# Performance work log

Hardware: AMD Instinct MI355X
Metric: run time of the kernel (lower is better)

The kernel has to match this reference:

```python
import jax, jax.numpy as jnp
import numpy as np

D_MODEL = 1024
HEADS = 16
HEAD_DIM = D_MODEL // HEADS


def setup_inputs() -> dict:
    key = jax.random.key(0)
    ks = jax.random.split(key, 6)
    B, S, D = 2, 2048, D_MODEL
    scale = 1.0 / np.sqrt(D)
    x = jax.random.normal(ks[0], (B, S, D), dtype=jnp.float32)
    mask = jax.random.randint(ks[1], (B, S), 0, 2, dtype=jnp.int32)
    Wq = jax.random.normal(ks[2], (D, D), dtype=jnp.float32) * scale
    Wk = jax.random.normal(ks[3], (D, D), dtype=jnp.float32) * scale
    Wv = jax.random.normal(ks[4], (D, D), dtype=jnp.float32) * scale
    Wp = jax.random.normal(ks[5], (D, D), dtype=jnp.float32) * scale
    zb = jnp.zeros((D,), dtype=jnp.float32)
    return {"x": x, "mask": mask, "Wq": Wq, "bq": zb, "Wk": Wk, "bk": zb,
            "Wv": Wv, "bv": zb, "Wp": Wp, "bp": zb}


def reference(x, mask, Wq, bq, Wk, bk, Wv, bv, Wp, bp):
    B, S, D = x.shape
    H, Dh = HEADS, HEAD_DIM

    def split_heads(t):  # [B,S,D] -> [B,H,S,Dh]
        return t.reshape(B, S, H, Dh).transpose(0, 2, 1, 3)

    q = split_heads(x @ Wq + bq)
    k = split_heads(x @ Wk + bk)
    v = split_heads(x @ Wv + bv)

    att = jnp.einsum('bhqd,bhkd->bhqk', q, k) / jnp.sqrt(jnp.float32(Dh))
    # key-padding mask: [B,S] -> [B,1,1,S]; masked positions -> -inf
    m = (mask[:, None, None, :] != 0)
    att = jnp.where(m, att, -jnp.inf)
    att = jax.nn.softmax(att, axis=-1)
    # rows that were fully masked produce NaN -> zero them (masked_fill(isnan, 0))
    att = jnp.where(jnp.isnan(att), 0.0, att)

    y = jnp.einsum('bhqk,bhkd->bhqd', att, v)  # [B,H,S,Dh]
    y = y.transpose(0, 2, 1, 3).reshape(B, S, D)
    return y @ Wp + bp
```

## Files before the change

### kernel.cpp

```cpp
#include <hip/hip_runtime.h>
#include <math.h>

#define D_MODEL 1024
#define HEADS 16
#define HEAD_DIM 64
#define SEQ 2048
#define BATCH 2
#define KVT 64
#define QTILE 128
#define SCALE_Q 0.18033688f

typedef __attribute__((ext_vector_type(8))) short bf16x8;
typedef __attribute__((ext_vector_type(4))) float f32x4;
typedef __attribute__((ext_vector_type(16))) float f32x16;

__device__ __forceinline__ short f2bf(float f) {
    union { float f; unsigned u; } v; v.f = f;
    unsigned r = (v.u + 0x7FFFu + ((v.u >> 16) & 1u)) >> 16;
    return (short)r;
}

__device__ __forceinline__ unsigned cvt_pk_bf16(float lo, float hi) {
    unsigned r;
    asm("v_cvt_pk_bf16_f32 %0, %1, %2" : "=v"(r) : "v"(lo), "v"(hi));
    return r;
}

__device__ __forceinline__ float fexp2(float x) {
    float r;
    asm("v_exp_f32 %0, %1" : "=v"(r) : "v"(x));
    return r;
}

__global__ __launch_bounds__(256) void prep(
    const float* __restrict__ x, const float* __restrict__ Wq,
    const float* __restrict__ Wk, const float* __restrict__ Wv,
    const float* __restrict__ Wp, const int* __restrict__ mask,
    short* __restrict__ xb, short* __restrict__ Wqkvt,
    short* __restrict__ Wpt, float* __restrict__ maskf) {
    __shared__ float t[32][33];
    const int bid = blockIdx.x;
    if (bid < 2048) {
        const int i = bid * 256 + threadIdx.x;
        float4 a = ((const float4*)x)[2 * i];
        float4 b = ((const float4*)x)[2 * i + 1];
        short r[8] = {f2bf(a.x), f2bf(a.y), f2bf(a.z), f2bf(a.w),
                      f2bf(b.x), f2bf(b.y), f2bf(b.z), f2bf(b.w)};
        *(uint4*)(xb + 8 * i) = *(uint4*)r;
    } else if (bid < 6144) {
        const int tt = bid - 2048;
        const int z = tt >> 10;
        const int rem = tt & 1023;
        const float* W = z == 0 ? Wq : z == 1 ? Wk : z == 2 ? Wv : Wp;
        short* dst = (z < 3) ? Wqkvt + (size_t)z * 1024 * 1024 : Wpt;
        const int n0 = (rem & 31) * 32, k0 = (rem >> 5) * 32;
        const int tx = threadIdx.x & 31, ty = threadIdx.x >> 5;
#pragma unroll
        for (int j = 0; j < 4; ++j)
            t[ty + j * 8][tx] = W[(size_t)(k0 + ty + j * 8) * 1024 + n0 + tx];
        __syncthreads();
#pragma unroll
        for (int j = 0; j < 4; ++j) {
            const int n = ty + j * 8;
            dst[(size_t)(n0 + n) * 1024 + k0 + tx] = f2bf(t[tx][n]);
        }
    } else {
        const int i = (bid - 6144) * 256 + threadIdx.x;
        maskf[i] = mask[i] ? 0.f : -INFINITY;
    }
}

template <int MODE>
__global__ __launch_bounds__(256) void mfma_gemm(
    const short* __restrict__ A, const short* __restrict__ Bt,
    const float* __restrict__ b0, const float* __restrict__ b1,
    const float* __restrict__ b2, float* __restrict__ outf,
    short* __restrict__ o0, short* __restrict__ o1, short* __restrict__ o2,
    int M, int N, int K) {
    __shared__ short As[2 * 128 * 32];
    __shared__ short Bs[2 * 128 * 32];

    const int tid = threadIdx.x;
    const int wave = tid >> 6, lane = tid & 63;
    const int l15 = lane & 15, lhi = lane >> 4;
    const int wm = wave >> 1, wn = wave & 1;
    const int bm0 = blockIdx.y * 128, bn0 = blockIdx.x * 128;

    f32x4 acc[4][4];
#pragma unroll
    for (int m = 0; m < 4; ++m)
#pragma unroll
        for (int n = 0; n < 4; ++n) acc[m][n] = (f32x4){0.f, 0.f, 0.f, 0.f};

#define STAGE_G(buf, kt_)                                                         \
    {                                                                             \
        const int k0 = (kt_) * 32;                                                \
        _Pragma("unroll") for (int p = 0; p < 2; ++p) {                           \
            const int o = (wave * 2 + p) * 64 + lane;                             \
            const int r = o >> 2;                                                 \
            const int gs = (o & 3) ^ ((r >> 1) & 3);                              \
            __builtin_amdgcn_global_load_lds(                                     \
                (const __attribute__((address_space(1))) void*)(                  \
                    A + (size_t)(bm0 + r) * K + k0 + gs * 8),                     \
                (__attribute__((address_space(3))) void*)(                        \
                    As + (size_t)(buf) * 4096 + (wave * 2 + p) * 512),            \
                16, 0, 0);                                                        \
            __builtin_amdgcn_global_load_lds(                                     \
                (const __attribute__((address_space(1))) void*)(                  \
                    Bt + (size_t)(bn0 + r) * K + k0 + gs * 8),                    \
                (__attribute__((address_space(3))) void*)(                        \
                    Bs + (size_t)(buf) * 4096 + (wave * 2 + p) * 512),            \
                16, 0, 0);                                                        \
        }                                                                         \
    }

    const int NT = K / 32;
    STAGE_G(0, 0);
    __syncthreads();
    for (int kt = 0; kt < NT; ++kt) {
        const int cur = kt & 1;
        if (kt + 1 < NT) STAGE_G((kt + 1) & 1, kt + 1);
        bf16x8 af[4], bf[4];
        const int sg = (lhi ^ ((l15 >> 1) & 3)) * 16;
#pragma unroll
        for (int m = 0; m < 4; ++m)
            af[m] = *(const bf16x8*)((char*)As + cur * 8192 +
                                     (wm * 64 + m * 16 + l15) * 64 + sg);
#pragma unroll
        for (int n = 0; n < 4; ++n)
            bf[n] = *(const bf16x8*)((char*)Bs + cur * 8192 +
                                     (wn * 64 + n * 16 + l15) * 64 + sg);
        __builtin_amdgcn_s_setprio(1);
#pragma unroll
        for (int m = 0; m < 4; ++m)
#pragma unroll
            for (int n = 0; n < 4; ++n)
                acc[m][n] = __builtin_amdgcn_mfma_f32_16x16x32_bf16(af[m], bf[n], acc[m][n], 0, 0, 0);
        __builtin_amdgcn_s_setprio(0);
        __syncthreads();
    }
#undef STAGE_G

    const int which = (MODE == 1) ? (bn0 >> 10) : 0;
#pragma unroll
    for (int m = 0; m < 4; ++m) {
#pragma unroll
        for (int n = 0; n < 4; ++n) {
            const int col = bn0 + wn * 64 + n * 16 + l15;
            if (MODE == 0) {
#pragma unroll
                for (int rr = 0; rr < 4; ++rr) {
                    const int row = bm0 + wm * 64 + m * 16 + lhi * 4 + rr;
                    outf[(size_t)row * N + col] = acc[m][n][rr] + b0[col];
                }
            } else {
                const int cc = col & 1023;
                const int h = cc >> 6, dh = cc & 63;
                const int row0 = bm0 + wm * 64 + m * 16 + lhi * 4;
                const int b = row0 >> 11, s0 = row0 & (SEQ - 1);
                if (which == 2) {
                    const float bias = b2[cc];
                    uint2 w;
                    w.x = cvt_pk_bf16(acc[m][n][0] + bias, acc[m][n][1] + bias);
                    w.y = cvt_pk_bf16(acc[m][n][2] + bias, acc[m][n][3] + bias);
                    *(uint2*)(o2 + ((size_t)(b * HEADS + h) * HEAD_DIM + dh) * SEQ + s0) = w;
                } else {
                    const float bias = (which == 0 ? b0 : b1)[cc];
                    short* dst = which == 0 ? o0 : o1;
#pragma unroll
                    for (int rr = 0; rr < 4; ++rr) {
                        float v = acc[m][n][rr] + bias;
                        if (which == 0) v *= SCALE_Q;
                        dst[(((size_t)(b * HEADS + h)) * SEQ + s0 + rr) * HEAD_DIM + dh] = f2bf(v);
                    }
                }
            }
        }
    }
}

__global__ __launch_bounds__(256, 3) void flash_attn(
    const short* __restrict__ Q, const short* __restrict__ K,
    const short* __restrict__ Vt, const float* __restrict__ maskf,
    short* __restrict__ Y) {
    __shared__ unsigned char kt[2][KVT * 128];
    __shared__ unsigned char vt[2][HEAD_DIM * 128];
    __shared__ unsigned char pb[4][32 * 128];

    const int tid = threadIdx.x;
    const int wave = tid >> 6;
    const int lane = tid & 63;
    const int l31 = lane & 31;
    const int lh = lane >> 5;

    const int nwg = gridDim.x;
    const int wg = blockIdx.x;
    const int swz = (wg & 7) * (nwg >> 3) + (wg >> 3);
    const int qt = swz & 15;
    const int bh = swz >> 4;
    const int b = bh >> 4;

    const int q0 = qt * QTILE + wave * 32;

    const short* Qp = Q + ((size_t)bh * SEQ + q0 + l31) * HEAD_DIM;
    bf16x8 qf[4];
#pragma unroll
    for (int s = 0; s < 4; ++s)
        qf[s] = *(const bf16x8*)(Qp + 16 * s + 8 * lh);

    const unsigned char* Kb8 = (const unsigned char*)(K + (size_t)bh * SEQ * HEAD_DIM);
    const unsigned char* Vb8 = (const unsigned char*)(Vt + (size_t)bh * HEAD_DIM * SEQ);
    const float* mb = maskf + b * SEQ;

#define STAGE(buf, kvi)                                                            \
    {                                                                              \
        const unsigned char* kbase = Kb8 + (size_t)(kvi) * KVT * 128;              \
        const unsigned char* vbase = Vb8 + (size_t)(kvi) * 128;                    \
        _Pragma("unroll") for (int p = 0; p < 2; ++p) {                            \
            const int g = wave * 2 + p;                                            \
            __builtin_amdgcn_global_load_lds(                                      \
                (const __attribute__((address_space(1))) void*)(                   \
                    kbase + lane * 128 + g * 16),                                  \
                (__attribute__((address_space(3))) void*)(&kt[buf][g * 1024]),     \
                16, 0, 0);                                                         \
            __builtin_amdgcn_global_load_lds(                                      \
                (const __attribute__((address_space(1))) void*)(                   \
                    vbase + (size_t)lane * (SEQ * 2) + g * 16),                    \
                (__attribute__((address_space(3))) void*)(&vt[buf][g * 1024]),     \
                16, 0, 0);                                                         \
        }                                                                          \
    }

    f32x16 accO[2];
    float mrow = -30000.f, lrow = 0.f;
#pragma unroll
    for (int d = 0; d < 2; ++d)
#pragma unroll
        for (int r = 0; r < 16; ++r) accO[d][r] = 0.f;

    STAGE(0, 0);
    __syncthreads();

    for (int kv = 0; kv < SEQ / KVT; ++kv) {
        const int cur = kv & 1;
        if (kv + 1 < SEQ / KVT) STAGE((kv + 1) & 1, kv + 1);

        const int k0 = kv * KVT;

        f32x16 accS[2];
#pragma unroll
        for (int kb = 0; kb < 2; ++kb)
#pragma unroll
            for (int r = 0; r < 16; ++r) accS[kb][r] = 0.f;
#pragma unroll
        for (int s = 0; s < 4; ++s) {
            bf16x8 kf[2];
#pragma unroll
            for (int kb = 0; kb < 2; ++kb)
                kf[kb] = *(const bf16x8*)(kt[cur] + (2 * s + lh) * 1024 +
                                          (32 * kb + l31) * 16);
            __builtin_amdgcn_s_setprio(1);
#pragma unroll
            for (int kb = 0; kb < 2; ++kb)
                accS[kb] = __builtin_amdgcn_mfma_f32_32x32x16_bf16(kf[kb], qf[s], accS[kb], 0, 0, 0);
            __builtin_amdgcn_s_setprio(0);
        }

#pragma unroll
        for (int kb = 0; kb < 2; ++kb)
#pragma unroll
            for (int g = 0; g < 4; ++g) {
                const f32x4 ma = *(const f32x4*)(mb + k0 + 32 * kb + 8 * g + 4 * lh);
#pragma unroll
                for (int j = 0; j < 4; ++j) accS[kb][4 * g + j] += ma[j];
            }

        float mx[2];
#pragma unroll
        for (int kb = 0; kb < 2; ++kb) {
            float a0 = fmaxf(fmaxf(accS[kb][0], accS[kb][1]), fmaxf(accS[kb][2], accS[kb][3]));
            float a1 = fmaxf(fmaxf(accS[kb][4], accS[kb][5]), fmaxf(accS[kb][6], accS[kb][7]));
            float a2 = fmaxf(fmaxf(accS[kb][8], accS[kb][9]), fmaxf(accS[kb][10], accS[kb][11]));
            float a3 = fmaxf(fmaxf(accS[kb][12], accS[kb][13]), fmaxf(accS[kb][14], accS[kb][15]));
            mx[kb] = fmaxf(fmaxf(a0, a1), fmaxf(a2, a3));
        }
        float smax = fmaxf(mx[0], mx[1]);
        smax = fmaxf(smax, __shfl_xor(smax, 32));

        if (!__all(smax <= mrow + 11.5f)) {
            const float mn = fmaxf(mrow, smax);
            const float alpha = fexp2(mrow - mn);
            lrow *= alpha;
#pragma unroll
            for (int d = 0; d < 2; ++d)
#pragma unroll
                for (int r = 0; r < 16; ++r) accO[d][r] *= alpha;
            mrow = mn;
        }

        float rs = 0.f;
#pragma unroll
        for (int kb = 0; kb < 2; ++kb)
#pragma unroll
            for (int r = 0; r < 16; ++r) {
                const float pv = fexp2(accS[kb][r] - mrow);
                accS[kb][r] = pv;
                rs += pv;
            }
        rs += __shfl_xor(rs, 32);
        lrow += rs;

#pragma unroll
        for (int kb = 0; kb < 2; ++kb)
#pragma unroll
            for (int g = 0; g < 4; ++g) {
                uint2 w;
                w.x = cvt_pk_bf16(accS[kb][4 * g], accS[kb][4 * g + 1]);
                w.y = cvt_pk_bf16(accS[kb][4 * g + 2], accS[kb][4 * g + 3]);
                *(uint2*)(pb[wave] + (4 * kb + g) * 512 + l31 * 16 + lh * 8) = w;
            }

#pragma unroll
        for (int t = 0; t < 4; ++t) {
            const bf16x8 pf = *(const bf16x8*)(pb[wave] + (2 * t + lh) * 512 + l31 * 16);
            bf16x8 vf[2];
#pragma unroll
            for (int db = 0; db < 2; ++db)
                vf[db] = *(const bf16x8*)(vt[cur] + (2 * t + lh) * 1024 +
                                          (32 * db + l31) * 16);
            __builtin_amdgcn_s_setprio(1);
#pragma unroll
            for (int db = 0; db < 2; ++db)
                accO[db] = __builtin_amdgcn_mfma_f32_32x32x16_bf16(vf[db], pf, accO[db], 0, 0, 0);
            __builtin_amdgcn_s_setprio(0);
        }
        __syncthreads();
    }
#undef STAGE

    const float inv = (lrow > 0.f) ? 1.f / lrow : 0.f;
    const int qg = q0 + l31;
    short* Yp = Y + ((size_t)b * SEQ + qg) * D_MODEL + (bh & 15) * HEAD_DIM;
#pragma unroll
    for (int db = 0; db < 2; ++db)
#pragma unroll
        for (int g = 0; g < 4; ++g) {
            uint2 w;
            w.x = cvt_pk_bf16(accO[db][4 * g] * inv, accO[db][4 * g + 1] * inv);
            w.y = cvt_pk_bf16(accO[db][4 * g + 2] * inv, accO[db][4 * g + 3] * inv);
            *(uint2*)(Yp + 32 * db + 8 * g + 4 * lh) = w;
        }
}

extern "C" void kernel_launch(void* const* d_in, const int* in_sizes, int n_in,
                              void* d_out, int out_size, void* d_ws, size_t ws_size,
                              hipStream_t stream) {
    const float* x    = (const float*)d_in[0];
    const int*   mask = (const int*)  d_in[1];
    const float* Wq   = (const float*)d_in[2];
    const float* bq   = (const float*)d_in[3];
    const float* Wk   = (const float*)d_in[4];
    const float* bk   = (const float*)d_in[5];
    const float* Wv   = (const float*)d_in[6];
    const float* bv   = (const float*)d_in[7];
    const float* Wp   = (const float*)d_in[8];
    const float* bp   = (const float*)d_in[9];
    float* out = (float*)d_out;

    short* ws    = (short*)d_ws;
    short* xb    = ws;
    short* Wqkvt = xb + ((size_t)4 << 20);
    short* Wpt   = Wqkvt + ((size_t)3 << 20);
    short* Qb    = Wpt + ((size_t)1 << 20);
    short* Kb    = Qb + ((size_t)4 << 20);
    short* Vtb   = Kb + ((size_t)4 << 20);
    short* Yb    = Vtb + ((size_t)4 << 20);
    float* maskf = (float*)(Yb + ((size_t)4 << 20));

    const int M = BATCH * SEQ;

    prep<<<dim3(6160), 256, 0, stream>>>(x, Wq, Wk, Wv, Wp, mask,
                                         xb, Wqkvt, Wpt, maskf);

    mfma_gemm<1><<<dim3(3 * D_MODEL / 128, M / 128), 256, 0, stream>>>(
        xb, Wqkvt, bq, bk, bv, nullptr, Qb, Kb, Vtb, M, 3 * D_MODEL, D_MODEL);

    flash_attn<<<dim3(BATCH * HEADS * (SEQ / QTILE)), 256, 0, stream>>>(Qb, Kb, Vtb, maskf, Yb);

    mfma_gemm<0><<<dim3(D_MODEL / 128, M / 128), 256, 0, stream>>>(
        Yb, Wpt, bp, bp, bp, out, nullptr, nullptr, nullptr, M, D_MODEL, D_MODEL);
}
```

Measured before the change: 143.8 us.

## Pre-swizzle K/V global layouts for contiguous LDS loads; pass P via lane shuffles

The QKV GEMM epilogue now writes K and V in chunked layouts of 8-element groups, so each wave's global_load_lds in the attention kernel reads contiguous 1 KB segments instead of strided rows. The P matrix fragment for the PV MFMA is now built from registers with a cross-half-wave shuffle instead of a round trip through a per-wave LDS buffer, which frees that LDS. The cost is scattered 2-byte stores for K in the GEMM epilogue and extra shuffle instructions per tile.

Result: slower. 171.4 us (+19.2%).

```diff
diff --git a/kernel.cpp b/kernel.cpp
--- a/kernel.cpp
+++ b/kernel.cpp
@@ -158,21 +158,26 @@
                 const int h = cc >> 6, dh = cc & 63;
                 const int row0 = bm0 + wm * 64 + m * 16 + lhi * 4;
                 const int b = row0 >> 11, s0 = row0 & (SEQ - 1);
+                const int bh = b * HEADS + h;
                 if (which == 2) {
                     const float bias = b2[cc];
                     uint2 w;
                     w.x = cvt_pk_bf16(acc[m][n][0] + bias, acc[m][n][1] + bias);
                     w.y = cvt_pk_bf16(acc[m][n][2] + bias, acc[m][n][3] + bias);
-                    *(uint2*)(o2 + ((size_t)(b * HEADS + h) * HEAD_DIM + dh) * SEQ + s0) = w;
+                    *(uint2*)(o2 + (((size_t)bh * 256 + (s0 >> 3)) * 64 + dh) * 8 +
+                              (s0 & 7)) = w;
+                } else if (which == 1) {
+                    const float bias = b1[cc];
+                    short* base = o1 + ((size_t)bh * 8 + (dh >> 3)) * (SEQ * 8) + (dh & 7);
+#pragma unroll
+                    for (int rr = 0; rr < 4; ++rr)
+                        base[(size_t)(s0 + rr) * 8] = f2bf(acc[m][n][rr] + bias);
                 } else {
-                    const float bias = (which == 0 ? b0 : b1)[cc];
-                    short* dst = which == 0 ? o0 : o1;
-#pragma unroll
-                    for (int rr = 0; rr < 4; ++rr) {
-                        float v = acc[m][n][rr] + bias;
-                        if (which == 0) v *= SCALE_Q;
-                        dst[(((size_t)(b * HEADS + h)) * SEQ + s0 + rr) * HEAD_DIM + dh] = f2bf(v);
-                    }
+                    const float bias = b0[cc];
+#pragma unroll
+                    for (int rr = 0; rr < 4; ++rr)
+                        o0[(((size_t)bh) * SEQ + s0 + rr) * HEAD_DIM + dh] =
+                            f2bf((acc[m][n][rr] + bias) * SCALE_Q);
                 }
             }
         }
@@ -180,12 +185,11 @@
 }
 
 __global__ __launch_bounds__(256, 3) void flash_attn(
-    const short* __restrict__ Q, const short* __restrict__ K,
-    const short* __restrict__ Vt, const float* __restrict__ maskf,
+    const short* __restrict__ Q, const short* __restrict__ Kg,
+    const short* __restrict__ Vg, const float* __restrict__ maskf,
     short* __restrict__ Y) {
     __shared__ unsigned char kt[2][KVT * 128];
     __shared__ unsigned char vt[2][HEAD_DIM * 128];
-    __shared__ unsigned char pb[4][32 * 128];
 
     const int tid = threadIdx.x;
     const int wave = tid >> 6;
@@ -208,24 +212,22 @@
     for (int s = 0; s < 4; ++s)
         qf[s] = *(const bf16x8*)(Qp + 16 * s + 8 * lh);
 
-    const unsigned char* Kb8 = (const unsigned char*)(K + (size_t)bh * SEQ * HEAD_DIM);
-    const unsigned char* Vb8 = (const unsigned char*)(Vt + (size_t)bh * HEAD_DIM * SEQ);
+    const unsigned char* Kb8 = (const unsigned char*)(Kg + (size_t)bh * 8 * SEQ * 8);
+    const unsigned char* Vb8 = (const unsigned char*)(Vg + (size_t)bh * 256 * 64 * 8);
     const float* mb = maskf + b * SEQ;
 
 #define STAGE(buf, kvi)                                                            \
     {                                                                              \
-        const unsigned char* kbase = Kb8 + (size_t)(kvi) * KVT * 128;              \
-        const unsigned char* vbase = Vb8 + (size_t)(kvi) * 128;                    \
         _Pragma("unroll") for (int p = 0; p < 2; ++p) {                            \
             const int g = wave * 2 + p;                                            \
             __builtin_amdgcn_global_load_lds(                                      \
                 (const __attribute__((address_space(1))) void*)(                   \
-                    kbase + lane * 128 + g * 16),                                  \
+                    Kb8 + ((size_t)g * SEQ + (kvi) * KVT) * 16 + lane * 16),       \
                 (__attribute__((address_space(3))) void*)(&kt[buf][g * 1024]),     \
                 16, 0, 0);                                                         \
             __builtin_amdgcn_global_load_lds(                                      \
                 (const __attribute__((address_space(1))) void*)(                   \
-                    vbase + (size_t)lane * (SEQ * 2) + g * 16),                    \
+                    Vb8 + ((size_t)((kvi) * 8 + g) * 64) * 16 + lane * 16),        \
                 (__attribute__((address_space(3))) void*)(&vt[buf][g * 1024]),     \
                 16, 0, 0);                                                         \
         }                                                                          \
@@ -299,30 +301,34 @@
         }
 
         float rs = 0.f;
+        uint2 w[8];
 #pragma unroll
         for (int kb = 0; kb < 2; ++kb)
 #pragma unroll
-            for (int r = 0; r < 16; ++r) {
-                const float pv = fexp2(accS[kb][r] - mrow);
-                accS[kb][r] = pv;
-                rs += pv;
+            for (int g = 0; g < 4; ++g) {
+                f32x4 p;
+#pragma unroll
+                for (int j = 0; j < 4; ++j) {
+                    p[j] = fexp2(accS[kb][4 * g + j] - mrow);
+                    rs += p[j];
+                }
+                w[4 * kb + g].x = cvt_pk_bf16(p[0], p[1]);
+                w[4 * kb + g].y = cvt_pk_bf16(p[2], p[3]);
             }
         rs += __shfl_xor(rs, 32);
         lrow += rs;
 
 #pragma unroll
-        for (int kb = 0; kb < 2; ++kb)
-#pragma unroll
-            for (int g = 0; g < 4; ++g) {
-                uint2 w;
-                w.x = cvt_pk_bf16(accS[kb][4 * g], accS[kb][4 * g + 1]);
-                w.y = cvt_pk_bf16(accS[kb][4 * g + 2], accS[kb][4 * g + 3]);
-                *(uint2*)(pb[wave] + (4 * kb + g) * 512 + l31 * 16 + lh * 8) = w;
-            }
-
-#pragma unroll
         for (int t = 0; t < 4; ++t) {
-            const bf16x8 pf = *(const bf16x8*)(pb[wave] + (2 * t + lh) * 512 + l31 * 16);
+            const uint2 mine = w[2 * t + lh];
+            const uint2 sendv = w[2 * t + 1 - lh];
+            uint2 recv;
+            recv.x = __shfl_xor(sendv.x, 32);
+            recv.y = __shfl_xor(sendv.y, 32);
+            union { bf16x8 v; uint2 u[2]; } pfu;
+            pfu.u[0] = lh ? recv : mine;
+            pfu.u[1] = lh ? mine : recv;
+            const bf16x8 pf = pfu.v;
             bf16x8 vf[2];
 #pragma unroll
             for (int db = 0; db < 2; ++db)
@@ -345,10 +351,10 @@
     for (int db = 0; db < 2; ++db)
 #pragma unroll
         for (int g = 0; g < 4; ++g) {
-            uint2 w;
-            w.x = cvt_pk_bf16(accO[db][4 * g] * inv, accO[db][4 * g + 1] * inv);
-            w.y = cvt_pk_bf16(accO[db][4 * g + 2] * inv, accO[db][4 * g + 3] * inv);
-            *(uint2*)(Yp + 32 * db + 8 * g + 4 * lh) = w;
+            uint2 w2;
+            w2.x = cvt_pk_bf16(accO[db][4 * g] * inv, accO[db][4 * g + 1] * inv);
+            w2.y = cvt_pk_bf16(accO[db][4 * g + 2] * inv, accO[db][4 * g + 3] * inv);
+            *(uint2*)(Yp + 32 * db + 8 * g + 4 * lh) = w2;
         }
 }
 
@@ -372,9 +378,9 @@
     short* Wqkvt = xb + ((size_t)4 << 20);
     short* Wpt   = Wqkvt + ((size_t)3 << 20);
     short* Qb    = Wpt + ((size_t)1 << 20);
-    short* Kb    = Qb + ((size_t)4 << 20);
-    short* Vtb   = Kb + ((size_t)4 << 20);
-    short* Yb    = Vtb + ((size_t)4 << 20);
+    short* Kgb   = Qb + ((size_t)4 << 20);
+    short* Vgb   = Kgb + ((size_t)4 << 20);
+    short* Yb    = Vgb + ((size_t)4 << 20);
     float* maskf = (float*)(Yb + ((size_t)4 << 20));
 
     const int M = BATCH * SEQ;
@@ -383,9 +389,9 @@
                                          xb, Wqkvt, Wpt, maskf);
 
     mfma_gemm<1><<<dim3(3 * D_MODEL / 128, M / 128), 256, 0, stream>>>(
-        xb, Wqkvt, bq, bk, bv, nullptr, Qb, Kb, Vtb, M, 3 * D_MODEL, D_MODEL);
-
-    flash_attn<<<dim3(BATCH * HEADS * (SEQ / QTILE)), 256, 0, stream>>>(Qb, Kb, Vtb, maskf, Yb);
+        xb, Wqkvt, bq, bk, bv, nullptr, Qb, Kgb, Vgb, M, 3 * D_MODEL, D_MODEL);
+
+    flash_attn<<<dim3(BATCH * HEADS * (SEQ / QTILE)), 256, 0, stream>>>(Qb, Kgb, Vgb, maskf, Yb);
 
     mfma_gemm<0><<<dim3(D_MODEL / 128, M / 128), 256, 0, stream>>>(
         Yb, Wpt, bp, bp, bp, out, nullptr, nullptr, nullptr, M, D_MODEL, D_MODEL);
```
